# Kernel tuning notes

Hardware: AMD Instinct MI355X
Metric: run time of the kernel (lower is better)

The kernel has to match this reference:

```python
import jax, jax.numpy as jnp
import numpy as np

B, DK, DV, TQ, TM, H, W = 4, 128, 512, 1, 2, 64, 64
NEG = -1e30  # effectively -inf for masked memory logits (avoids NaN in softmax)


def setup_inputs() -> dict:
    key = jax.random.key(0)
    ks = jax.random.split(key, 6)
    qkey = jax.random.normal(ks[0], (B, DK, TQ, H, W), dtype=jnp.float32)
    qval = jax.random.normal(ks[1], (B, DV, TQ, H, W), dtype=jnp.float32)
    qmask = jax.random.bernoulli(ks[2], 0.5, (B, 1, TQ, H, W))
    mkey = jax.random.normal(ks[3], (B, DK, TM, H, W), dtype=jnp.float32)
    mval = jax.random.normal(ks[4], (B, DV, TM, H, W), dtype=jnp.float32)
    mmask = jax.random.bernoulli(ks[5], 0.5, (B, 1, TM, H, W))
    return {"qkey": qkey, "qval": qval, "qmask": qmask,
            "mkey": mkey, "mval": mval, "mmask": mmask}


def reference(qkey, qval, qmask, mkey, mval, mmask):
    b, dk = qkey.shape[:2]
    dv = qval.shape[1]
    qk = qkey.reshape(b, dk, -1)          # [B, Dk, Nq]
    qv = qval.reshape(b, dv, -1)          # [B, Dv, Nq]
    qm = qmask.reshape(b, -1)             # [B, Nq] bool
    mk = mkey.reshape(b, dk, -1)          # [B, Dk, Nm]
    mv = mval.reshape(b, dv, -1)          # [B, Dv, Nm]
    mm = mmask.reshape(b, -1)             # [B, Nm] bool

    # logits over memory positions for every query position
    logits = jnp.einsum('bdm,bdq->bmq', mk, qk) / jnp.sqrt(jnp.asarray(dk, qk.dtype))
    logits = jnp.where(mm[:, :, None], logits, NEG)  # exclude unmasked memory
    p = jax.nn.softmax(logits, axis=1)               # softmax over memory dim
    read = jnp.einsum('bdm,bmq->bdq', mv, p)         # [B, Dv, Nq]

    # only masked query positions are updated; skip batches with empty masks
    valid = (qm.any(axis=1) & mm.any(axis=1))[:, None, None]
    read = jnp.where(valid & qm[:, None, :], read, jnp.zeros((), read.dtype))
    return (qv + read).reshape(qval.shape)
```

## Files before the change

kernel.cpp:

```cpp
#include <hip/hip_runtime.h>
#include <stdint.h>

#define NB 4
#define DK 128
#define DV 512
#define NQ 4096
#define NM 8192
#define SCALE 0.08838834764831845f
#define LOG2E 1.4426950408889634f

typedef unsigned short u16;
typedef __attribute__((ext_vector_type(8))) short short8;
typedef __attribute__((ext_vector_type(4))) float f32x4;

typedef __attribute__((address_space(1))) const uint32_t* as1_u32p;
typedef __attribute__((address_space(3))) uint32_t* as3_u32p;
__device__ __forceinline__ void gld16(const void* g, void* l){
  __builtin_amdgcn_global_load_lds((as1_u32p)g, (as3_u32p)l, 16, 0, 0);
}

template<int D, int N, int SWZ>
__global__ void k_tconv(const float* __restrict__ in, u16* __restrict__ out, float scale){
  const int tilesN = N / 64;
  int id = blockIdx.x;
  int b  = id / ((D/64) * tilesN);
  int r  = id % ((D/64) * tilesN);
  int dt = r / tilesN, nt = r % tilesN;
  const float* inb = in + (size_t)b * D * N;
  u16* outb = out + (size_t)b * N * D;
  __shared__ float tile[64][65];
  int c  = threadIdx.x & 63;
  int r4 = threadIdx.x >> 6;
#pragma unroll
  for (int rr = 0; rr < 16; ++rr){
    int row = rr * 4 + r4;
    tile[row][c] = inb[(size_t)(dt*64 + row) * N + nt*64 + c] * scale;
  }
  __syncthreads();
  int h   = threadIdx.x & 31;
  int nl0 = threadIdx.x >> 5;
#pragma unroll
  for (int rr = 0; rr < 8; ++rr){
    int n  = rr * 8 + nl0;
    int ng = nt*64 + n;
    unsigned lo = __float_as_uint(tile[2*h][n]);
    unsigned hi = __float_as_uint(tile[2*h+1][n]);
    unsigned plo = (lo + 0x7fffu + ((lo >> 16) & 1u)) >> 16;
    unsigned phi = (hi + 0x7fffu + ((hi >> 16) & 1u)) & 0xffff0000u;
    int d = dt*64 + 2*h;
    if (SWZ) d ^= ((ng & 7) << 3);
    *(unsigned*)&outb[(size_t)ng * D + d] = phi | plo;
  }
}

__global__ void k_conv(const float* __restrict__ in, u16* __restrict__ out, int n4){
  int i = blockIdx.x * blockDim.x + threadIdx.x;
  int stride = gridDim.x * blockDim.x;
  const float4* in4 = (const float4*)in;
  uint2* out2 = (uint2*)out;
  for (; i < n4; i += stride){
    float4 v = in4[i];
    unsigned ux = __float_as_uint(v.x), uy = __float_as_uint(v.y);
    unsigned uz = __float_as_uint(v.z), uw = __float_as_uint(v.w);
    uint2 o;
    o.x = (((uy + 0x7fffu + ((uy>>16)&1u)) & 0xffff0000u)) | ((ux + 0x7fffu + ((ux>>16)&1u)) >> 16);
    o.y = (((uw + 0x7fffu + ((uw>>16)&1u)) & 0xffff0000u)) | ((uz + 0x7fffu + ((uz>>16)&1u)) >> 16);
    out2[i] = o;
  }
}

__global__ void k_valid(const int* __restrict__ qm, const int* __restrict__ mm,
                        int* __restrict__ valid, float* __restrict__ mmF){
  int b = blockIdx.x;
  int anyq = 0, anym = 0;
  for (int i = threadIdx.x; i < NQ; i += 256) anyq |= qm[b*NQ + i];
  for (int i = threadIdx.x; i < NM; i += 256){
    int v = mm[b*NM + i];
    anym |= v;
    mmF[(size_t)b*NM + i] = v ? 1.0f : 0.0f;
  }
  __shared__ int sh[256];
  sh[threadIdx.x] = ((anyq != 0) ? 1 : 0) | ((anym != 0) ? 2 : 0);
  __syncthreads();
  for (int s = 128; s > 0; s >>= 1){
    if (threadIdx.x < s) sh[threadIdx.x] |= sh[threadIdx.x + s];
    __syncthreads();
  }
  if (threadIdx.x == 0) valid[b] = ((sh[0] & 1) && (sh[0] & 2)) ? 1 : 0;
}

__global__ __launch_bounds__(256, 2) void k_attn(
    const u16* __restrict__ qkT,
    const u16* __restrict__ mkTs,
    const u16* __restrict__ mvB,
    const float* __restrict__ qval,
    const int* __restrict__ qmask,
    const float* __restrict__ mmF,
    const int* __restrict__ validf,
    float* __restrict__ out)
{
  __shared__ u16 lds_k[2][64][128];
  __shared__ u16 lds_pT[64][72];
  __shared__ float lds_l[64];

  int tid = threadIdx.x;
  int bid = blockIdx.x;
  int lid = ((bid & 7) << 6) | (bid >> 3);
  int b   = lid >> 7;
  int rem = lid & 127;
  int qb  = rem >> 1, dvh = rem & 1;
  int q0  = qb << 6, dv0 = dvh << 8;
  int w = tid >> 6, lane = tid & 63, g = lane >> 4, lr = lane & 15;

  const u16* qkTb = qkT + (size_t)b * NQ * DK;
  const u16* mkTb = mkTs + (size_t)b * NM * DK;
  const u16* mvBb = mvB + (size_t)b * DV * NM;
  const float* mmFb = mmF + (size_t)b * NM;

  int qs = q0 + w * 16;
  short8 qfrag[4];
#pragma unroll
  for (int ks = 0; ks < 4; ++ks)
    qfrag[ks] = *(const short8*)&qkTb[(size_t)(qs + lr) * DK + ks*32 + g*8];

  const u16* vrow[4];
#pragma unroll
  for (int df = 0; df < 4; ++df)
    vrow[df] = mvBb + (size_t)(dv0 + w*64 + df*16 + lr) * NM;

  f32x4 acc[4][4];
#pragma unroll
  for (int i = 0; i < 4; ++i)
#pragma unroll
    for (int j = 0; j < 4; ++j)
      acc[i][j] = (f32x4){0.f, 0.f, 0.f, 0.f};
  float lrun = 0.f;

  int ldsoff_w = __builtin_amdgcn_readfirstlane(w * 4096);
  int lane16 = lane * 16;
  int swz = (lr & 7) << 3;

  {
    const char* s = (const char*)mkTb;
    char* l0 = (char*)&lds_k[0][0][0];
#pragma unroll
    for (int i = 0; i < 4; ++i)
      gld16(s + ldsoff_w + i*1024 + lane16, l0 + ldsoff_w + i*1024);
  }

  for (int mt = 0; mt < NM/64; ++mt){
    int m0 = mt << 6;
    const u16* lk = &lds_k[mt & 1][0][0];
    __syncthreads();
    if (mt + 1 < NM/64){
      const char* s = (const char*)(mkTb + (size_t)(mt + 1) * (64 * DK));
      char* l1 = (char*)&lds_k[(mt + 1) & 1][0][0];
#pragma unroll
      for (int i = 0; i < 4; ++i)
        gld16(s + ldsoff_w + i*1024 + lane16, l1 + ldsoff_w + i*1024);
    }
    short8 vf[4][2];
#pragma unroll
    for (int df = 0; df < 4; ++df)
#pragma unroll
      for (int k2 = 0; k2 < 2; ++k2)
        vf[df][k2] = *(const short8*)&vrow[df][m0 + k2*32 + g*8];

    f32x4 sfr[4];
#pragma unroll
    for (int mf = 0; mf < 4; ++mf){
      f32x4 c = (f32x4){0.f, 0.f, 0.f, 0.f};
#pragma unroll
      for (int ks = 0; ks < 4; ++ks){
        const short8 a = *(const short8*)&lk[(mf*16 + lr) * 128 + ((ks*32 + g*8) ^ swz)];
        c = __builtin_amdgcn_mfma_f32_16x16x32_bf16(a, qfrag[ks], c, 0, 0, 0);
      }
      sfr[mf] = c;
    }

    float tsum = 0.f;
#pragma unroll
    for (int mf = 0; mf < 4; ++mf){
      float4 mk4 = *(const float4*)&mmFb[m0 + mf*16 + g*4];
      float p0 = mk4.x * exp2f(sfr[mf][0]);
      float p1 = mk4.y * exp2f(sfr[mf][1]);
      float p2 = mk4.z * exp2f(sfr[mf][2]);
      float p3 = mk4.w * exp2f(sfr[mf][3]);
      sfr[mf][0] = p0; sfr[mf][1] = p1; sfr[mf][2] = p2; sfr[mf][3] = p3;
      tsum += (p0 + p1) + (p2 + p3);
    }
    tsum += __shfl_xor(tsum, 16, 64);
    tsum += __shfl_xor(tsum, 32, 64);
    lrun += tsum;

#pragma unroll
    for (int mf = 0; mf < 4; ++mf){
      unsigned u0 = __float_as_uint(sfr[mf][0]);
      unsigned u1 = __float_as_uint(sfr[mf][1]);
      unsigned u2 = __float_as_uint(sfr[mf][2]);
      unsigned u3 = __float_as_uint(sfr[mf][3]);
      uint2 pk;
      pk.x = (u1 & 0xffff0000u) | (u0 >> 16);
      pk.y = (u3 & 0xffff0000u) | (u2 >> 16);
      *(uint2*)&lds_pT[w*16 + lr][mf*16 + g*4] = pk;
    }
    __syncthreads();

#pragma unroll
    for (int qf = 0; qf < 4; ++qf){
#pragma unroll
      for (int k2 = 0; k2 < 2; ++k2){
        const short8 pf = *(const short8*)&lds_pT[qf*16 + lr][k2*32 + g*8];
#pragma unroll
        for (int df = 0; df < 4; ++df)
          acc[df][qf] = __builtin_amdgcn_mfma_f32_16x16x32_bf16(vf[df][k2], pf, acc[df][qf], 0, 0, 0);
      }
    }
  }

  if (g == 0) lds_l[w*16 + lr] = lrun;
  __syncthreads();
  int vb = validf[b];
  const int* qmb = qmask + (size_t)b * NQ;
  const float* qvb = qval + (size_t)b * DV * NQ;
  float* outb = out + (size_t)b * DV * NQ;
#pragma unroll
  for (int qf = 0; qf < 4; ++qf){
    int q = q0 + qf*16 + lr;
    float l_ = lds_l[qf*16 + lr];
    float rl = (l_ > 0.f) ? 1.0f / l_ : 0.f;
    float gate = (vb && qmb[q]) ? rl : 0.f;
#pragma unroll
    for (int df = 0; df < 4; ++df){
#pragma unroll
      for (int r = 0; r < 4; ++r){
        int dv = dv0 + w*64 + df*16 + g*4 + r;
        size_t idx = (size_t)dv * NQ + q;
        outb[idx] = qvb[idx] + acc[df][qf][r] * gate;
      }
    }
  }
}

extern "C" void kernel_launch(void* const* d_in, const int* in_sizes, int n_in,
                              void* d_out, int out_size, void* d_ws, size_t ws_size,
                              hipStream_t stream) {
  const float* qkey  = (const float*)d_in[0];
  const float* qval  = (const float*)d_in[1];
  const int*   qmask = (const int*)d_in[2];
  const float* mkey  = (const float*)d_in[3];
  const float* mval  = (const float*)d_in[4];
  const int*   mmask = (const int*)d_in[5];
  float* out = (float*)d_out;

  char* ws = (char*)d_ws;
  u16* qkT = (u16*)(ws);
  u16* mkT = (u16*)(ws + (size_t)4*1024*1024);
  u16* mvB = (u16*)(ws + (size_t)12*1024*1024);
  float* mmF = (float*)(ws + (size_t)44*1024*1024);
  int* validf = (int*)(ws + (size_t)44*1024*1024 + (size_t)NB*NM*4);

  k_tconv<DK, NQ, 0><<<dim3(NB * (DK/64) * (NQ/64)), dim3(256), 0, stream>>>(qkey, qkT, SCALE * LOG2E);
  k_tconv<DK, NM, 1><<<dim3(NB * (DK/64) * (NM/64)), dim3(256), 0, stream>>>(mkey, mkT, 1.0f);
  k_conv<<<dim3(4096), dim3(256), 0, stream>>>(mval, mvB, NB*DV*NM/4);
  k_valid<<<dim3(NB), dim3(256), 0, stream>>>(qmask, mmask, validf, mmF);
  k_attn<<<dim3(512), dim3(256), 0, stream>>>(qkT, mkT, mvB, qval, qmask, mmF, validf, out);
}
```

Baseline: 586.8 us.

## Fuse prep kernels and split attention across more blocks with higher occupancy

Merges the four preprocessing kernels into one launch that dispatches on block index, removing three launch overheads. The attention kernel now splits DV into four chunks instead of two, doubling the grid to 1024 blocks with half the accumulators per thread, and raises launch bounds to allow four blocks per CU. It also swizzles the P-transpose LDS layout to avoid bank conflicts and hoists the mask loads ahead of the QK MFMAs. The cost is that every block recomputes QK^T and the softmax for twice as many DV chunks, doubling the score work and K-tile traffic.

```diff
diff --git a/kernel.cpp b/kernel.cpp
--- a/kernel.cpp
+++ b/kernel.cpp
@@ -19,16 +19,16 @@
   __builtin_amdgcn_global_load_lds((as1_u32p)g, (as3_u32p)l, 16, 0, 0);
 }
 
+
 template<int D, int N, int SWZ>
-__global__ void k_tconv(const float* __restrict__ in, u16* __restrict__ out, float scale){
+__device__ void tconv_body(const float* __restrict__ in, u16* __restrict__ out,
+                           float scale, int id, float (*tile)[65]){
   const int tilesN = N / 64;
-  int id = blockIdx.x;
   int b  = id / ((D/64) * tilesN);
   int r  = id % ((D/64) * tilesN);
   int dt = r / tilesN, nt = r % tilesN;
   const float* inb = in + (size_t)b * D * N;
   u16* outb = out + (size_t)b * N * D;
-  __shared__ float tile[64][65];
   int c  = threadIdx.x & 63;
   int r4 = threadIdx.x >> 6;
 #pragma unroll
@@ -53,9 +53,10 @@
   }
 }
 
-__global__ void k_conv(const float* __restrict__ in, u16* __restrict__ out, int n4){
-  int i = blockIdx.x * blockDim.x + threadIdx.x;
-  int stride = gridDim.x * blockDim.x;
+__device__ void conv_body(const float* __restrict__ in, u16* __restrict__ out,
+                          int n4, int bb, int nblk){
+  int i = bb * 256 + threadIdx.x;
+  int stride = nblk * 256;
   const float4* in4 = (const float4*)in;
   uint2* out2 = (uint2*)out;
   for (; i < n4; i += stride){
@@ -69,9 +70,9 @@
   }
 }
 
-__global__ void k_valid(const int* __restrict__ qm, const int* __restrict__ mm,
-                        int* __restrict__ valid, float* __restrict__ mmF){
-  int b = blockIdx.x;
+__device__ void valid_body(const int* __restrict__ qm, const int* __restrict__ mm,
+                           int* __restrict__ valid, float* __restrict__ mmF,
+                           int b, int* sh){
   int anyq = 0, anym = 0;
   for (int i = threadIdx.x; i < NQ; i += 256) anyq |= qm[b*NQ + i];
   for (int i = threadIdx.x; i < NM; i += 256){
@@ -79,7 +80,6 @@
     anym |= v;
     mmF[(size_t)b*NM + i] = v ? 1.0f : 0.0f;
   }
-  __shared__ int sh[256];
   sh[threadIdx.x] = ((anyq != 0) ? 1 : 0) | ((anym != 0) ? 2 : 0);
   __syncthreads();
   for (int s = 128; s > 0; s >>= 1){
@@ -89,7 +89,30 @@
   if (threadIdx.x == 0) valid[b] = ((sh[0] & 1) && (sh[0] & 2)) ? 1 : 0;
 }
 
-__global__ __launch_bounds__(256, 2) void k_attn(
+#define PREP_A (NB * (DK/64) * (NQ/64))
+#define PREP_B (NB * (DK/64) * (NM/64))
+#define PREP_C 2048
+#define PREP_D NB
+
+__global__ void k_prep(const float* __restrict__ qkey, const float* __restrict__ mkey,
+                       const float* __restrict__ mval,
+                       const int* __restrict__ qmask, const int* __restrict__ mmask,
+                       u16* __restrict__ qkT, u16* __restrict__ mkT, u16* __restrict__ mvB,
+                       float* __restrict__ mmF, int* __restrict__ validf){
+  __shared__ float tile[64][65];
+  int bb = blockIdx.x;
+  if (bb < PREP_A){
+    tconv_body<DK, NQ, 0>(qkey, qkT, SCALE * LOG2E, bb, tile);
+  } else if (bb < PREP_A + PREP_B){
+    tconv_body<DK, NM, 1>(mkey, mkT, 1.0f, bb - PREP_A, tile);
+  } else if (bb < PREP_A + PREP_B + PREP_C){
+    conv_body(mval, mvB, NB*DV*NM/4, bb - PREP_A - PREP_B, PREP_C);
+  } else {
+    valid_body(qmask, mmask, validf, mmF, bb - PREP_A - PREP_B - PREP_C, (int*)tile);
+  }
+}
+
+__global__ __launch_bounds__(256, 4) void k_attn(
     const u16* __restrict__ qkT,
     const u16* __restrict__ mkTs,
     const u16* __restrict__ mvB,
@@ -99,17 +122,17 @@
     const int* __restrict__ validf,
     float* __restrict__ out)
 {
-  __shared__ u16 lds_k[2][64][128];
-  __shared__ u16 lds_pT[64][72];
-  __shared__ float lds_l[64];
+  __shared__ uint4 arena4[2560];
+  char* arena = (char*)arena4;
+  u16* pT = (u16*)(arena + 32768);
 
   int tid = threadIdx.x;
   int bid = blockIdx.x;
-  int lid = ((bid & 7) << 6) | (bid >> 3);
-  int b   = lid >> 7;
-  int rem = lid & 127;
-  int qb  = rem >> 1, dvh = rem & 1;
-  int q0  = qb << 6, dv0 = dvh << 8;
+  int lid = ((bid & 7) << 7) | (bid >> 3);
+  int b   = lid >> 8;
+  int rem = lid & 255;
+  int qb  = rem >> 2, dq = rem & 3;
+  int q0  = qb << 6, dv0 = dq << 7;
   int w = tid >> 6, lane = tid & 63, g = lane >> 4, lr = lane & 15;
 
   const u16* qkTb = qkT + (size_t)b * NQ * DK;
@@ -123,14 +146,14 @@
   for (int ks = 0; ks < 4; ++ks)
     qfrag[ks] = *(const short8*)&qkTb[(size_t)(qs + lr) * DK + ks*32 + g*8];
 
-  const u16* vrow[4];
-#pragma unroll
-  for (int df = 0; df < 4; ++df)
-    vrow[df] = mvBb + (size_t)(dv0 + w*64 + df*16 + lr) * NM;
-
-  f32x4 acc[4][4];
-#pragma unroll
-  for (int i = 0; i < 4; ++i)
+  const u16* vrow[2];
+#pragma unroll
+  for (int df = 0; df < 2; ++df)
+    vrow[df] = mvBb + (size_t)(dv0 + w*32 + df*16 + lr) * NM;
+
+  f32x4 acc[2][4];
+#pragma unroll
+  for (int i = 0; i < 2; ++i)
 #pragma unroll
     for (int j = 0; j < 4; ++j)
       acc[i][j] = (f32x4){0.f, 0.f, 0.f, 0.f};
@@ -138,33 +161,37 @@
 
   int ldsoff_w = __builtin_amdgcn_readfirstlane(w * 4096);
   int lane16 = lane * 16;
-  int swz = (lr & 7) << 3;
+  int swzK = (lr & 7) << 3;
+  int swzP = (lr & 7) << 1;
 
   {
     const char* s = (const char*)mkTb;
-    char* l0 = (char*)&lds_k[0][0][0];
 #pragma unroll
     for (int i = 0; i < 4; ++i)
-      gld16(s + ldsoff_w + i*1024 + lane16, l0 + ldsoff_w + i*1024);
+      gld16(s + ldsoff_w + i*1024 + lane16, arena + ldsoff_w + i*1024);
   }
 
   for (int mt = 0; mt < NM/64; ++mt){
     int m0 = mt << 6;
-    const u16* lk = &lds_k[mt & 1][0][0];
+    const u16* lk = (const u16*)(arena + ((mt & 1) << 14));
     __syncthreads();
     if (mt + 1 < NM/64){
       const char* s = (const char*)(mkTb + (size_t)(mt + 1) * (64 * DK));
-      char* l1 = (char*)&lds_k[(mt + 1) & 1][0][0];
+      char* l1 = arena + (((mt + 1) & 1) << 14);
 #pragma unroll
       for (int i = 0; i < 4; ++i)
         gld16(s + ldsoff_w + i*1024 + lane16, l1 + ldsoff_w + i*1024);
     }
-    short8 vf[4][2];
-#pragma unroll
-    for (int df = 0; df < 4; ++df)
+    short8 vf[2][2];
+#pragma unroll
+    for (int df = 0; df < 2; ++df)
 #pragma unroll
       for (int k2 = 0; k2 < 2; ++k2)
         vf[df][k2] = *(const short8*)&vrow[df][m0 + k2*32 + g*8];
+    float4 mk4v[4];
+#pragma unroll
+    for (int mf = 0; mf < 4; ++mf)
+      mk4v[mf] = *(const float4*)&mmFb[m0 + mf*16 + g*4];
 
     f32x4 sfr[4];
 #pragma unroll
@@ -172,7 +199,7 @@
       f32x4 c = (f32x4){0.f, 0.f, 0.f, 0.f};
 #pragma unroll
       for (int ks = 0; ks < 4; ++ks){
-        const short8 a = *(const short8*)&lk[(mf*16 + lr) * 128 + ((ks*32 + g*8) ^ swz)];
+        const short8 a = *(const short8*)&lk[(mf*16 + lr) * 128 + ((ks*32 + g*8) ^ swzK)];
         c = __builtin_amdgcn_mfma_f32_16x16x32_bf16(a, qfrag[ks], c, 0, 0, 0);
       }
       sfr[mf] = c;
@@ -181,11 +208,10 @@
     float tsum = 0.f;
 #pragma unroll
     for (int mf = 0; mf < 4; ++mf){
-      float4 mk4 = *(const float4*)&mmFb[m0 + mf*16 + g*4];
-      float p0 = mk4.x * exp2f(sfr[mf][0]);
-      float p1 = mk4.y * exp2f(sfr[mf][1]);
-      float p2 = mk4.z * exp2f(sfr[mf][2]);
-      float p3 = mk4.w * exp2f(sfr[mf][3]);
+      float p0 = mk4v[mf].x * exp2f(sfr[mf][0]);
+      float p1 = mk4v[mf].y * exp2f(sfr[mf][1]);
+      float p2 = mk4v[mf].z * exp2f(sfr[mf][2]);
+      float p3 = mk4v[mf].w * exp2f(sfr[mf][3]);
       sfr[mf][0] = p0; sfr[mf][1] = p1; sfr[mf][2] = p2; sfr[mf][3] = p3;
       tsum += (p0 + p1) + (p2 + p3);
     }
@@ -193,6 +219,7 @@
     tsum += __shfl_xor(tsum, 32, 64);
     lrun += tsum;
 
+    int prow = w*16 + lr;
 #pragma unroll
     for (int mf = 0; mf < 4; ++mf){
       unsigned u0 = __float_as_uint(sfr[mf][0]);
@@ -202,22 +229,27 @@
       uint2 pk;
       pk.x = (u1 & 0xffff0000u) | (u0 >> 16);
       pk.y = (u3 & 0xffff0000u) | (u2 >> 16);
-      *(uint2*)&lds_pT[w*16 + lr][mf*16 + g*4] = pk;
+      int gr = (4*mf + g) ^ swzP;
+      *(uint2*)&pT[prow*64 + gr*4] = pk;
     }
     __syncthreads();
 
 #pragma unroll
     for (int qf = 0; qf < 4; ++qf){
+      int rrow = qf*16 + lr;
+      int rswz = (lr & 7) << 1;
 #pragma unroll
       for (int k2 = 0; k2 < 2; ++k2){
-        const short8 pf = *(const short8*)&lds_pT[qf*16 + lr][k2*32 + g*8];
-#pragma unroll
-        for (int df = 0; df < 4; ++df)
+        int gr = (8*k2 + 2*g) ^ rswz;
+        const short8 pf = *(const short8*)&pT[rrow*64 + gr*4];
+#pragma unroll
+        for (int df = 0; df < 2; ++df)
           acc[df][qf] = __builtin_amdgcn_mfma_f32_16x16x32_bf16(vf[df][k2], pf, acc[df][qf], 0, 0, 0);
       }
     }
   }
 
+  float* lds_l = (float*)arena;
   if (g == 0) lds_l[w*16 + lr] = lrun;
   __syncthreads();
   int vb = validf[b];
@@ -231,10 +263,10 @@
     float rl = (l_ > 0.f) ? 1.0f / l_ : 0.f;
     float gate = (vb && qmb[q]) ? rl : 0.f;
 #pragma unroll
-    for (int df = 0; df < 4; ++df){
+    for (int df = 0; df < 2; ++df){
 #pragma unroll
       for (int r = 0; r < 4; ++r){
-        int dv = dv0 + w*64 + df*16 + g*4 + r;
+        int dv = dv0 + w*32 + df*16 + g*4 + r;
         size_t idx = (size_t)dv * NQ + q;
         outb[idx] = qvb[idx] + acc[df][qf][r] * gate;
       }
@@ -260,9 +292,7 @@
   float* mmF = (float*)(ws + (size_t)44*1024*1024);
   int* validf = (int*)(ws + (size_t)44*1024*1024 + (size_t)NB*NM*4);
 
-  k_tconv<DK, NQ, 0><<<dim3(NB * (DK/64) * (NQ/64)), dim3(256), 0, stream>>>(qkey, qkT, SCALE * LOG2E);
-  k_tconv<DK, NM, 1><<<dim3(NB * (DK/64) * (NM/64)), dim3(256), 0, stream>>>(mkey, mkT, 1.0f);
-  k_conv<<<dim3(4096), dim3(256), 0, stream>>>(mval, mvB, NB*DV*NM/4);
-  k_valid<<<dim3(NB), dim3(256), 0, stream>>>(qmask, mmask, validf, mmF);
-  k_attn<<<dim3(512), dim3(256), 0, stream>>>(qkT, mkT, mvB, qval, qmask, mmF, validf, out);
-}
+  k_prep<<<dim3(PREP_A + PREP_B + PREP_C + PREP_D), dim3(256), 0, stream>>>(
+      qkey, mkey, mval, qmask, mmask, qkT, mkT, mvB, mmF, validf);
+  k_attn<<<dim3(1024), dim3(256), 0, stream>>>(qkT, mkT, mvB, qval, qmask, mmF, validf, out);
+}
```

Result: slower. 617.2 us (+5.2%).
